# Optimization experiments

Hardware: AMD Instinct MI355X
Metric: run time of the kernel (lower is better)

## Reference

```python
import jax, jax.numpy as jnp
import numpy as np

K = 3
TEMPERATURE = 0.07
THRESHOLD = 0.5


def setup_inputs() -> dict:
    key = jax.random.key(0)
    kA, kB = jax.random.split(key)
    A = jax.random.normal(kA, (8, 32, 128, 128), dtype=jnp.float32)
    B = jax.random.normal(kB, (8, 32, 128, 128), dtype=jnp.float32)
    return {"A": A, "B": B}


def _l2_normalize(x, axis=1, eps=1e-12):
    # matches torch F.normalize(p=2): x / max(||x||, eps)
    n = jnp.sqrt(jnp.sum(x * x, axis=axis, keepdims=True))
    return x / jnp.maximum(n, eps)


def _unfold(x, k):
    # x: [B, C, H, W] -> patches [B, C, k*k, H, W], zero-padded (like nn.Unfold)
    b, c, h, w = x.shape
    pad = k // 2
    xp = jnp.pad(x, ((0, 0), (0, 0), (pad, pad), (pad, pad)))
    views = [xp[:, :, di:di + h, dj:dj + w] for di in range(k) for dj in range(k)]
    return jnp.stack(views, axis=2)


def reference(A, B):
    An = _l2_normalize(A, axis=1)
    Bn = _l2_normalize(B, axis=1)
    patches = _unfold(Bn, K)                      # [B, C, k*k, H, W]
    sim = jnp.einsum('bchw,bckhw->bkhw', An, patches)  # [B, k*k, H, W]
    labels = (sim > THRESHOLD).astype(sim.dtype)  # hard labels, no grad path
    log_prob = jax.nn.log_softmax(sim / TEMPERATURE, axis=1)
    # per-pixel: -mean_b sum_k labels*log_prob; averaged over H*W pixels
    return -jnp.mean(jnp.sum(labels * log_prob, axis=1))
```

## Files before the change

kernel.cpp:

```cpp
#include <hip/hip_runtime.h>

namespace {
constexpr int Cc   = 32;
constexpr int H    = 128;
constexpr int W    = 128;
constexpr int HWsz = H * W;
constexpr int NPIX = 8 * HWsz;
constexpr int NROW = NPIX / W;
constexpr int CPG  = 8;
}

__device__ inline float2 mk2(float a, float b) { float2 r; r.x = a; r.y = b; return r; }
__device__ inline void fma2(float2& acc, const float2& a, const float2& b) {
    acc.x += a.x * b.x; acc.y += a.y * b.y;
}
__device__ inline void add2(float2& acc, const float2& v) { acc.x += v.x; acc.y += v.y; }

__global__ __launch_bounds__(256) void cl_fused_kernel(const float* __restrict__ A,
                                                       const float* __restrict__ B,
                                                       double* __restrict__ partial) {
    __shared__ float2 ls[13][192];

    int t   = threadIdx.x & 63;
    int g   = threadIdx.x >> 6;
    int blk = blockIdx.x;
    int b   = blk & 7;
    int h   = blk >> 3;
    int w0  = t * 2;

    int hc[3];
#pragma unroll
    for (int r = 0; r < 3; ++r) hc[r] = min(max(h + r - 1, 0), H - 1);

    const float* Ap  = A + (size_t)b * Cc * HWsz + (size_t)g * CPG * HWsz + h * W + w0;
    const float* Bg  = B + (size_t)b * Cc * HWsz + (size_t)g * CPG * HWsz;
    const float* Br0 = Bg + hc[0] * W + w0;
    const float* Br1 = Bg + hc[1] * W + w0;
    const float* Br2 = Bg + hc[2] * W + w0;

    float2 sim[9], bn[3];
#pragma unroll
    for (int k = 0; k < 9; ++k) sim[k] = mk2(0, 0);
#pragma unroll
    for (int r = 0; r < 3; ++r) bn[r] = mk2(0, 0);
    float2 sa2 = mk2(0, 0);

#pragma unroll
    for (int c = 0; c < CPG; ++c) {
        float2 a2 = *(const float2*)(Ap  + c * HWsz);
        float2 b0 = *(const float2*)(Br0 + c * HWsz);
        float2 b1 = *(const float2*)(Br1 + c * HWsz);
        float2 b2 = *(const float2*)(Br2 + c * HWsz);
        float l0 = __shfl_up(b0.y, 1, 64), r0 = __shfl_down(b0.x, 1, 64);
        float l1 = __shfl_up(b1.y, 1, 64), r1 = __shfl_down(b1.x, 1, 64);
        float l2 = __shfl_up(b2.y, 1, 64), r2 = __shfl_down(b2.x, 1, 64);
        fma2(sa2, a2, a2);
        fma2(bn[0], b0, b0);
        fma2(bn[1], b1, b1);
        fma2(bn[2], b2, b2);
        fma2(sim[0], a2, mk2(l0, b0.x));
        fma2(sim[1], a2, b0);
        fma2(sim[2], a2, mk2(b0.y, r0));
        fma2(sim[3], a2, mk2(l1, b1.x));
        fma2(sim[4], a2, b1);
        fma2(sim[5], a2, mk2(b1.y, r1));
        fma2(sim[6], a2, mk2(l2, b2.x));
        fma2(sim[7], a2, b2);
        fma2(sim[8], a2, mk2(b2.y, r2));
    }

    if (g != 0) {
        int idx = (g - 1) * 64 + t;
#pragma unroll
        for (int k = 0; k < 9; ++k) ls[k][idx] = sim[k];
        ls[9][idx]  = bn[0];
        ls[10][idx] = bn[1];
        ls[11][idx] = bn[2];
        ls[12][idx] = sa2;
    }
    __syncthreads();

    if (g == 0) {
#pragma unroll
        for (int gg = 0; gg < 3; ++gg) {
            int idx = gg * 64 + t;
#pragma unroll
            for (int k = 0; k < 9; ++k) add2(sim[k], ls[k][idx]);
            add2(bn[0], ls[9][idx]);
            add2(bn[1], ls[10][idx]);
            add2(bn[2], ls[11][idx]);
            add2(sa2,   ls[12][idx]);
        }

        float2 rn[3]; float rlf[3], rrt[3];
#pragma unroll
        for (int r = 0; r < 3; ++r) {
            rn[r].x = 1.0f / fmaxf(sqrtf(bn[r].x), 1e-12f);
            rn[r].y = 1.0f / fmaxf(sqrtf(bn[r].y), 1e-12f);
            rlf[r] = __shfl_up(rn[r].y, 1, 64);
            rrt[r] = __shfl_down(rn[r].x, 1, 64);
        }

        float accf = 0.f;
#pragma unroll
        for (int j = 0; j < 2; ++j) {
            float ra = 1.0f / fmaxf(sqrtf(j == 0 ? sa2.x : sa2.y), 1e-12f);
            float lg[9], sv[9];
#pragma unroll
            for (int r = 0; r < 3; ++r) {
                bool vr_ = ((unsigned)(h + r - 1) < (unsigned)H);
                float nl = (j == 0) ? rlf[r]  : rn[r].x;
                float nm = (j == 0) ? rn[r].x : rn[r].y;
                float nr = (j == 0) ? rn[r].y : rrt[r];
                bool vl  = vr_ && (j == 1 || t > 0);
                bool vrg = vr_ && (j == 0 || t < 63);
                float s0v = (j == 0) ? sim[r * 3 + 0].x : sim[r * 3 + 0].y;
                float s1v = (j == 0) ? sim[r * 3 + 1].x : sim[r * 3 + 1].y;
                float s2v = (j == 0) ? sim[r * 3 + 2].x : sim[r * 3 + 2].y;
                float s0 = vl  ? s0v * ra * nl : 0.f;
                float s1 = vr_ ? s1v * ra * nm : 0.f;
                float s2 = vrg ? s2v * ra * nr : 0.f;
                sv[r * 3 + 0] = s0; lg[r * 3 + 0] = s0 / 0.07f;
                sv[r * 3 + 1] = s1; lg[r * 3 + 1] = s1 / 0.07f;
                sv[r * 3 + 2] = s2; lg[r * 3 + 2] = s2 / 0.07f;
            }
            float m = -1e30f;
#pragma unroll
            for (int k = 0; k < 9; ++k) m = fmaxf(m, lg[k]);
            float Z = 0.f;
#pragma unroll
            for (int k = 0; k < 9; ++k) Z += expf(lg[k] - m);
            float lZ = logf(Z);
#pragma unroll
            for (int k = 0; k < 9; ++k)
                if (sv[k] > 0.5f) accf += (m + lZ - lg[k]);
        }

        double acc = (double)accf;
#pragma unroll
        for (int s = 32; s > 0; s >>= 1) acc += __shfl_down(acc, s, 64);
        if (t == 0) partial[blk] = acc;
    }
}

__global__ __launch_bounds__(256) void cl_final_kernel(const double* __restrict__ partial,
                                                       float* __restrict__ out) {
    __shared__ double sd[256];
    double acc = 0.0;
    for (int i = threadIdx.x; i < NROW; i += 256) acc += partial[i];
    sd[threadIdx.x] = acc;
    __syncthreads();
    for (int s = 128; s > 0; s >>= 1) {
        if (threadIdx.x < s) sd[threadIdx.x] += sd[threadIdx.x + s];
        __syncthreads();
    }
    if (threadIdx.x == 0) out[0] = (float)(sd[0] / (double)NPIX);
}

extern "C" void kernel_launch(void* const* d_in, const int* in_sizes, int n_in,
                              void* d_out, int out_size, void* d_ws, size_t ws_size,
                              hipStream_t stream) {
    const float* A = (const float*)d_in[0];
    const float* B = (const float*)d_in[1];
    float* out = (float*)d_out;

    double* partial = (double*)d_ws;

    cl_fused_kernel<<<NROW, 256, 0, stream>>>(A, B, partial);
    cl_final_kernel<<<1, 256, 0, stream>>>(partial, out);
}
```

Baseline: 16.55 us.

## Use single-wave blocks with register double-buffered channel loads instead of LDS reduction

Each block now runs one 64-thread wavefront that walks all 32 channels itself, prefetching the next group of 4 channels into registers while the current group is processed. This removes the shared-memory partial-sum exchange and the barrier between four wavefronts. In exchange each row gets 4x fewer threads in flight, which cuts memory-level parallelism per row and raises register pressure from the prefetch buffers.

```diff
diff --git a/kernel.cpp b/kernel.cpp
--- a/kernel.cpp
+++ b/kernel.cpp
@@ -7,22 +7,18 @@
 constexpr int HWsz = H * W;
 constexpr int NPIX = 8 * HWsz;
 constexpr int NROW = NPIX / W;
-constexpr int CPG  = 8;
+constexpr int CG   = 4;
 }
 
 __device__ inline float2 mk2(float a, float b) { float2 r; r.x = a; r.y = b; return r; }
 __device__ inline void fma2(float2& acc, const float2& a, const float2& b) {
     acc.x += a.x * b.x; acc.y += a.y * b.y;
 }
-__device__ inline void add2(float2& acc, const float2& v) { acc.x += v.x; acc.y += v.y; }
 
-__global__ __launch_bounds__(256) void cl_fused_kernel(const float* __restrict__ A,
-                                                       const float* __restrict__ B,
-                                                       double* __restrict__ partial) {
-    __shared__ float2 ls[13][192];
-
-    int t   = threadIdx.x & 63;
-    int g   = threadIdx.x >> 6;
+__global__ __launch_bounds__(64, 4) void cl_fused_kernel(const float* __restrict__ A,
+                                                         const float* __restrict__ B,
+                                                         double* __restrict__ partial) {
+    int t   = threadIdx.x;
     int blk = blockIdx.x;
     int b   = blk & 7;
     int h   = blk >> 3;
@@ -32,11 +28,11 @@
 #pragma unroll
     for (int r = 0; r < 3; ++r) hc[r] = min(max(h + r - 1, 0), H - 1);
 
-    const float* Ap  = A + (size_t)b * Cc * HWsz + (size_t)g * CPG * HWsz + h * W + w0;
-    const float* Bg  = B + (size_t)b * Cc * HWsz + (size_t)g * CPG * HWsz;
-    const float* Br0 = Bg + hc[0] * W + w0;
-    const float* Br1 = Bg + hc[1] * W + w0;
-    const float* Br2 = Bg + hc[2] * W + w0;
+    const float* Ap  = A + (size_t)b * Cc * HWsz + h * W + w0;
+    const float* Bb  = B + (size_t)b * Cc * HWsz;
+    const float* Br0 = Bb + hc[0] * W + w0;
+    const float* Br1 = Bb + hc[1] * W + w0;
+    const float* Br2 = Bb + hc[2] * W + w0;
 
     float2 sim[9], bn[3];
 #pragma unroll
@@ -45,102 +41,98 @@
     for (int r = 0; r < 3; ++r) bn[r] = mk2(0, 0);
     float2 sa2 = mk2(0, 0);
 
+    float2 a_[2][CG], b0_[2][CG], b1_[2][CG], b2_[2][CG];
 #pragma unroll
-    for (int c = 0; c < CPG; ++c) {
-        float2 a2 = *(const float2*)(Ap  + c * HWsz);
-        float2 b0 = *(const float2*)(Br0 + c * HWsz);
-        float2 b1 = *(const float2*)(Br1 + c * HWsz);
-        float2 b2 = *(const float2*)(Br2 + c * HWsz);
-        float l0 = __shfl_up(b0.y, 1, 64), r0 = __shfl_down(b0.x, 1, 64);
-        float l1 = __shfl_up(b1.y, 1, 64), r1 = __shfl_down(b1.x, 1, 64);
-        float l2 = __shfl_up(b2.y, 1, 64), r2 = __shfl_down(b2.x, 1, 64);
-        fma2(sa2, a2, a2);
-        fma2(bn[0], b0, b0);
-        fma2(bn[1], b1, b1);
-        fma2(bn[2], b2, b2);
-        fma2(sim[0], a2, mk2(l0, b0.x));
-        fma2(sim[1], a2, b0);
-        fma2(sim[2], a2, mk2(b0.y, r0));
-        fma2(sim[3], a2, mk2(l1, b1.x));
-        fma2(sim[4], a2, b1);
-        fma2(sim[5], a2, mk2(b1.y, r1));
-        fma2(sim[6], a2, mk2(l2, b2.x));
-        fma2(sim[7], a2, b2);
-        fma2(sim[8], a2, mk2(b2.y, r2));
+    for (int c = 0; c < CG; ++c) {
+        a_[0][c]  = *(const float2*)(Ap  + c * HWsz);
+        b0_[0][c] = *(const float2*)(Br0 + c * HWsz);
+        b1_[0][c] = *(const float2*)(Br1 + c * HWsz);
+        b2_[0][c] = *(const float2*)(Br2 + c * HWsz);
     }
 
-    if (g != 0) {
-        int idx = (g - 1) * 64 + t;
 #pragma unroll
-        for (int k = 0; k < 9; ++k) ls[k][idx] = sim[k];
-        ls[9][idx]  = bn[0];
-        ls[10][idx] = bn[1];
-        ls[11][idx] = bn[2];
-        ls[12][idx] = sa2;
+    for (int cg = 0; cg < 8; ++cg) {
+        const int cur = cg & 1, nxt = cur ^ 1;
+        if (cg < 7) {
+            const int cb = (cg + 1) * CG;
+#pragma unroll
+            for (int c = 0; c < CG; ++c) {
+                a_[nxt][c]  = *(const float2*)(Ap  + (cb + c) * HWsz);
+                b0_[nxt][c] = *(const float2*)(Br0 + (cb + c) * HWsz);
+                b1_[nxt][c] = *(const float2*)(Br1 + (cb + c) * HWsz);
+                b2_[nxt][c] = *(const float2*)(Br2 + (cb + c) * HWsz);
+            }
+        }
+#pragma unroll
+        for (int c = 0; c < CG; ++c) {
+            float2 a2 = a_[cur][c], b0 = b0_[cur][c], b1 = b1_[cur][c], b2 = b2_[cur][c];
+            float l0 = __shfl_up(b0.y, 1, 64), r0 = __shfl_down(b0.x, 1, 64);
+            float l1 = __shfl_up(b1.y, 1, 64), r1 = __shfl_down(b1.x, 1, 64);
+            float l2 = __shfl_up(b2.y, 1, 64), r2 = __shfl_down(b2.x, 1, 64);
+            fma2(sa2, a2, a2);
+            fma2(bn[0], b0, b0);
+            fma2(bn[1], b1, b1);
+            fma2(bn[2], b2, b2);
+            fma2(sim[0], a2, mk2(l0, b0.x));
+            fma2(sim[1], a2, b0);
+            fma2(sim[2], a2, mk2(b0.y, r0));
+            fma2(sim[3], a2, mk2(l1, b1.x));
+            fma2(sim[4], a2, b1);
+            fma2(sim[5], a2, mk2(b1.y, r1));
+            fma2(sim[6], a2, mk2(l2, b2.x));
+            fma2(sim[7], a2, b2);
+            fma2(sim[8], a2, mk2(b2.y, r2));
+        }
     }
-    __syncthreads();
 
-    if (g == 0) {
+    float2 rn[3]; float rlf[3], rrt[3];
 #pragma unroll
-        for (int gg = 0; gg < 3; ++gg) {
-            int idx = gg * 64 + t;
+    for (int r = 0; r < 3; ++r) {
+        rn[r].x = 1.0f / fmaxf(sqrtf(bn[r].x), 1e-12f);
+        rn[r].y = 1.0f / fmaxf(sqrtf(bn[r].y), 1e-12f);
+        rlf[r] = __shfl_up(rn[r].y, 1, 64);
+        rrt[r] = __shfl_down(rn[r].x, 1, 64);
+    }
+
+    float accf = 0.f;
 #pragma unroll
-            for (int k = 0; k < 9; ++k) add2(sim[k], ls[k][idx]);
-            add2(bn[0], ls[9][idx]);
-            add2(bn[1], ls[10][idx]);
-            add2(bn[2], ls[11][idx]);
-            add2(sa2,   ls[12][idx]);
-        }
-
-        float2 rn[3]; float rlf[3], rrt[3];
+    for (int j = 0; j < 2; ++j) {
+        float ra = 1.0f / fmaxf(sqrtf(j == 0 ? sa2.x : sa2.y), 1e-12f);
+        float lg[9], sv[9];
 #pragma unroll
         for (int r = 0; r < 3; ++r) {
-            rn[r].x = 1.0f / fmaxf(sqrtf(bn[r].x), 1e-12f);
-            rn[r].y = 1.0f / fmaxf(sqrtf(bn[r].y), 1e-12f);
-            rlf[r] = __shfl_up(rn[r].y, 1, 64);
-            rrt[r] = __shfl_down(rn[r].x, 1, 64);
+            bool vr_ = ((unsigned)(h + r - 1) < (unsigned)H);
+            float nl = (j == 0) ? rlf[r]  : rn[r].x;
+            float nm = (j == 0) ? rn[r].x : rn[r].y;
+            float nr = (j == 0) ? rn[r].y : rrt[r];
+            bool vl  = vr_ && (j == 1 || t > 0);
+            bool vrg = vr_ && (j == 0 || t < 63);
+            float s0v = (j == 0) ? sim[r * 3 + 0].x : sim[r * 3 + 0].y;
+            float s1v = (j == 0) ? sim[r * 3 + 1].x : sim[r * 3 + 1].y;
+            float s2v = (j == 0) ? sim[r * 3 + 2].x : sim[r * 3 + 2].y;
+            float s0 = vl  ? s0v * ra * nl : 0.f;
+            float s1 = vr_ ? s1v * ra * nm : 0.f;
+            float s2 = vrg ? s2v * ra * nr : 0.f;
+            sv[r * 3 + 0] = s0; lg[r * 3 + 0] = s0 / 0.07f;
+            sv[r * 3 + 1] = s1; lg[r * 3 + 1] = s1 / 0.07f;
+            sv[r * 3 + 2] = s2; lg[r * 3 + 2] = s2 / 0.07f;
         }
+        float m = -1e30f;
+#pragma unroll
+        for (int k = 0; k < 9; ++k) m = fmaxf(m, lg[k]);
+        float Z = 0.f;
+#pragma unroll
+        for (int k = 0; k < 9; ++k) Z += expf(lg[k] - m);
+        float lZ = logf(Z);
+#pragma unroll
+        for (int k = 0; k < 9; ++k)
+            if (sv[k] > 0.5f) accf += (m + lZ - lg[k]);
+    }
 
-        float accf = 0.f;
+    double acc = (double)accf;
 #pragma unroll
-        for (int j = 0; j < 2; ++j) {
-            float ra = 1.0f / fmaxf(sqrtf(j == 0 ? sa2.x : sa2.y), 1e-12f);
-            float lg[9], sv[9];
-#pragma unroll
-            for (int r = 0; r < 3; ++r) {
-                bool vr_ = ((unsigned)(h + r - 1) < (unsigned)H);
-                float nl = (j == 0) ? rlf[r]  : rn[r].x;
-                float nm = (j == 0) ? rn[r].x : rn[r].y;
-                float nr = (j == 0) ? rn[r].y : rrt[r];
-                bool vl  = vr_ && (j == 1 || t > 0);
-                bool vrg = vr_ && (j == 0 || t < 63);
-                float s0v = (j == 0) ? sim[r * 3 + 0].x : sim[r * 3 + 0].y;
-                float s1v = (j == 0) ? sim[r * 3 + 1].x : sim[r * 3 + 1].y;
-                float s2v = (j == 0) ? sim[r * 3 + 2].x : sim[r * 3 + 2].y;
-                float s0 = vl  ? s0v * ra * nl : 0.f;
-                float s1 = vr_ ? s1v * ra * nm : 0.f;
-                float s2 = vrg ? s2v * ra * nr : 0.f;
-                sv[r * 3 + 0] = s0; lg[r * 3 + 0] = s0 / 0.07f;
-                sv[r * 3 + 1] = s1; lg[r * 3 + 1] = s1 / 0.07f;
-                sv[r * 3 + 2] = s2; lg[r * 3 + 2] = s2 / 0.07f;
-            }
-            float m = -1e30f;
-#pragma unroll
-            for (int k = 0; k < 9; ++k) m = fmaxf(m, lg[k]);
-            float Z = 0.f;
-#pragma unroll
-            for (int k = 0; k < 9; ++k) Z += expf(lg[k] - m);
-            float lZ = logf(Z);
-#pragma unroll
-            for (int k = 0; k < 9; ++k)
-                if (sv[k] > 0.5f) accf += (m + lZ - lg[k]);
-        }
-
-        double acc = (double)accf;
-#pragma unroll
-        for (int s = 32; s > 0; s >>= 1) acc += __shfl_down(acc, s, 64);
-        if (t == 0) partial[blk] = acc;
-    }
+    for (int s = 32; s > 0; s >>= 1) acc += __shfl_down(acc, s, 64);
+    if (t == 0) partial[blk] = acc;
 }
 
 __global__ __launch_bounds__(256) void cl_final_kernel(const double* __restrict__ partial,
@@ -166,6 +158,6 @@
 
     double* partial = (double*)d_ws;
 
-    cl_fused_kernel<<<NROW, 256, 0, stream>>>(A, B, partial);
+    cl_fused_kernel<<<NROW, 64, 0, stream>>>(A, B, partial);
     cl_final_kernel<<<1, 256, 0, stream>>>(partial, out);
 }
```

Result: slower. 31.66 us (+91.3%).
